# Optimization experiments

Hardware: AMD Instinct MI355X
Metric: run time of the kernel (lower is better)

Reference implementation:

```python
import jax, jax.numpy as jnp
import numpy as np

N_NODES = 50000
N_EDGES = 800000
IN_DIM = 768
HID = 32
HEADS = 4
OUT_DIM = 128


def setup_inputs() -> dict:
    key = jax.random.key(0)
    ks = jax.random.split(key, 7)
    h = jax.random.normal(ks[0], (N_NODES, IN_DIM), dtype=jnp.float32)
    W1 = jax.random.normal(ks[1], (HEADS, IN_DIM, HID), dtype=jnp.float32) * (1.0 / np.sqrt(IN_DIM))
    a1 = jax.random.normal(ks[2], (HEADS, 2 * HID), dtype=jnp.float32) * (1.0 / np.sqrt(2 * HID))
    W2 = jax.random.normal(ks[3], (1, HEADS * HID, OUT_DIM), dtype=jnp.float32) * (1.0 / np.sqrt(HEADS * HID))
    a2 = jax.random.normal(ks[4], (1, 2 * OUT_DIM), dtype=jnp.float32) * (1.0 / np.sqrt(2 * OUT_DIM))
    src = jax.random.randint(ks[5], (N_EDGES,), 0, N_NODES, dtype=jnp.int32)
    dst = jax.random.randint(ks[6], (N_EDGES,), 0, N_NODES, dtype=jnp.int32)
    return {"h": h, "W1": W1, "a1": a1, "W2": W2, "a2": a2, "src": src, "dst": dst}


def gat_layer(h, W, a, src, dst, n_nodes):
    # W: [H, Din, D], a: [H, 2D]; returns concat of heads: [N, H*D]
    z = jnp.einsum('ni,hio->nho', h, W)          # [N, H, D]
    D = z.shape[-1]
    a_src, a_dst = a[:, :D], a[:, D:]
    s_src = jnp.einsum('nhd,hd->nh', z, a_src)   # [N, H]
    s_dst = jnp.einsum('nhd,hd->nh', z, a_dst)
    e = jax.nn.leaky_relu(s_src[src] + s_dst[dst], 0.01)  # [E, H]
    # edge softmax over incoming edges of each dst node
    e_max = jax.ops.segment_max(e, dst, num_segments=n_nodes)
    e_max = jnp.where(jnp.isfinite(e_max), e_max, 0.0)     # empty segments -> -inf
    ex = jnp.exp(e - e_max[dst])
    denom = jax.ops.segment_sum(ex, dst, num_segments=n_nodes)
    alpha = ex / jnp.maximum(denom[dst], 1e-9)             # [E, H]
    msg = alpha[:, :, None] * z[src]                       # [E, H, D]
    out = jax.ops.segment_sum(msg, dst, num_segments=n_nodes)  # [N, H, D]
    return out.reshape(n_nodes, -1)


def reference(h, W1, a1, W2, a2, src, dst):
    n = h.shape[0]
    h1 = jax.nn.elu(gat_layer(h, W1, a1, src, dst, n))   # [N, HEADS*HID]
    h2 = gat_layer(h1, W2, a2, src, dst, n)              # [N, OUT_DIM]
    return h2
```

## Files before the change

### kernel.cpp

```cpp
#include <hip/hip_runtime.h>

#define NN 50000
#define NE 800000
#define IND 768
#define CH  128
#define NBLK 196
#define GBM 64
#define GBK 32
#define MBLKS 782

typedef __attribute__((ext_vector_type(8))) short bf16x8;
typedef __attribute__((ext_vector_type(4))) float f32x4;

__device__ __forceinline__ unsigned short bf16_rne(float f) {
    unsigned u = __float_as_uint(f);
    u += 0x7fffu + ((u >> 16) & 1u);
    return (unsigned short)(u >> 16);
}
__device__ __forceinline__ float bf16_to_f(unsigned short b) {
    return __uint_as_float(((unsigned)b) << 16);
}

__device__ __forceinline__ void cvt_split_pk(const float4& u0, const float4& u1,
                                             uint4& hi, uint4& lo)
{
    unsigned h0, h1, h2, h3;
    asm("v_cvt_pk_bf16_f32 %0, %1, %2" : "=v"(h0) : "v"(u0.x), "v"(u0.y));
    asm("v_cvt_pk_bf16_f32 %0, %1, %2" : "=v"(h1) : "v"(u0.z), "v"(u0.w));
    asm("v_cvt_pk_bf16_f32 %0, %1, %2" : "=v"(h2) : "v"(u1.x), "v"(u1.y));
    asm("v_cvt_pk_bf16_f32 %0, %1, %2" : "=v"(h3) : "v"(u1.z), "v"(u1.w));
    const float l0 = u0.x - __uint_as_float(h0 << 16);
    const float l1 = u0.y - __uint_as_float(h0 & 0xffff0000u);
    const float l2 = u0.z - __uint_as_float(h1 << 16);
    const float l3 = u0.w - __uint_as_float(h1 & 0xffff0000u);
    const float l4 = u1.x - __uint_as_float(h2 << 16);
    const float l5 = u1.y - __uint_as_float(h2 & 0xffff0000u);
    const float l6 = u1.z - __uint_as_float(h3 << 16);
    const float l7 = u1.w - __uint_as_float(h3 & 0xffff0000u);
    unsigned g0, g1, g2, g3;
    asm("v_cvt_pk_bf16_f32 %0, %1, %2" : "=v"(g0) : "v"(l0), "v"(l1));
    asm("v_cvt_pk_bf16_f32 %0, %1, %2" : "=v"(g1) : "v"(l2), "v"(l3));
    asm("v_cvt_pk_bf16_f32 %0, %1, %2" : "=v"(g2) : "v"(l4), "v"(l5));
    asm("v_cvt_pk_bf16_f32 %0, %1, %2" : "=v"(g3) : "v"(l6), "v"(l7));
    hi = make_uint4(h0, h1, h2, h3);
    lo = make_uint4(g0, g1, g2, g3);
}

__global__ void prep_b1(const float* __restrict__ W1,
                        unsigned short* __restrict__ Bhi, unsigned short* __restrict__ Blo)
{
    int idx = blockIdx.x * blockDim.x + threadIdx.x;
    if (idx >= CH * IND) return;
    int n = idx / IND, k = idx % IND;
    float v = W1[(size_t)(n >> 5) * IND * 32 + (size_t)k * 32 + (n & 31)];
    int kt = k >> 5, kk = k & 31, j = kk >> 3, e = kk & 7;
    int g = n * 4 + (j ^ ((n >> 1) & 3));
    int off = kt * 4096 + g * 8 + e;
    unsigned short hi = bf16_rne(v);
    float lo = v - bf16_to_f(hi);
    Bhi[off] = hi;
    Blo[off] = bf16_rne(lo);
}

__global__ void prep_b2(const float* __restrict__ W2,
                        unsigned short* __restrict__ Bhi, unsigned short* __restrict__ Blo)
{
    int idx = blockIdx.x * blockDim.x + threadIdx.x;
    if (idx >= CH * CH) return;
    int n = idx / CH, k = idx % CH;
    float v = W2[(size_t)k * CH + n];
    int kt = k >> 5, kk = k & 31, j = kk >> 3, e = kk & 7;
    int g = n * 4 + (j ^ ((n >> 1) & 3));
    int off = kt * 4096 + g * 8 + e;
    unsigned short hi = bf16_rne(v);
    float lo = v - bf16_to_f(hi);
    Bhi[off] = hi;
    Blo[off] = bf16_rne(lo);
}

template<int H>
__global__ __launch_bounds__(256) void gemm_fused(
    const float* __restrict__ A,
    const unsigned short* __restrict__ Bthi, const unsigned short* __restrict__ Btlo,
    const float* __restrict__ av,
    unsigned short* __restrict__ Z16,
    float* __restrict__ ss, float* __restrict__ sd, int K)
{
    __shared__ unsigned short Ahi[2048];
    __shared__ unsigned short Alo[2048];
    __shared__ unsigned short Bs[2][4096];
    __shared__ float sred[2][64][2];

    const int t = threadIdx.x;
    const int lane = t & 63;
    const int w = t >> 6;
    const int wr = w >> 1, wc = w & 1;
    const int lrow = lane & 15, kg = lane >> 4;
    const int m0 = blockIdx.x * GBM;
    const int nt = K >> 5;

    const int ar = t >> 2, aj = t & 3;
    const bool avalid = (m0 + ar) < NN;
    const float* aptr = A + (size_t)(avalid ? (m0 + ar) : 0) * K + aj * 8;
    const int ag8 = (ar * 4 + (aj ^ ((ar >> 1) & 3))) * 8;

    int aoff[2];
    #pragma unroll
    for (int mi = 0; mi < 2; ++mi) {
        const int r = wr * 32 + mi * 16 + lrow;
        aoff[mi] = (r * 4 + (kg ^ ((r >> 1) & 3))) * 8;
    }
    int boff[4];
    #pragma unroll
    for (int ni = 0; ni < 4; ++ni) {
        const int n = wc * 64 + ni * 16 + lrow;
        boff[ni] = (n * 4 + (kg ^ ((n >> 1) & 3))) * 8;
    }

    f32x4 acc[2][4];
    #pragma unroll
    for (int i = 0; i < 2; ++i)
        #pragma unroll
        for (int j = 0; j < 4; ++j) acc[i][j] = (f32x4)(0.f);

    for (int kt = 0; kt < nt; ++kt) {
        float4 v0 = make_float4(0.f, 0.f, 0.f, 0.f);
        float4 v1 = make_float4(0.f, 0.f, 0.f, 0.f);
        if (avalid) {
            const float* p = aptr + kt * GBK;
            v0 = *(const float4*)p;
            v1 = *(const float4*)(p + 4);
        }
        uint4 hi, lo;
        cvt_split_pk(v0, v1, hi, lo);
        __syncthreads();
        *(uint4*)&Ahi[ag8] = hi;
        *(uint4*)&Alo[ag8] = lo;
        #pragma unroll
        for (int i = 0; i < 4; ++i) {
            const int c = w * 4 + i;
            const int plane = c >> 3;
            const int co = (c & 7) * 512;
            const unsigned short* gs =
                (plane ? Btlo : Bthi) + (size_t)kt * 4096 + co + lane * 8;
            __builtin_amdgcn_global_load_lds(
                (const __attribute__((address_space(1))) unsigned int*)gs,
                (__attribute__((address_space(3))) unsigned int*)&Bs[plane][co],
                16, 0, 0);
        }
        __syncthreads();

        bf16x8 ahi[2], alo[2];
        #pragma unroll
        for (int mi = 0; mi < 2; ++mi) {
            ahi[mi] = *(const bf16x8*)&Ahi[aoff[mi]];
            alo[mi] = *(const bf16x8*)&Alo[aoff[mi]];
        }
        #pragma unroll
        for (int ni = 0; ni < 4; ++ni) {
            const bf16x8 bhi = *(const bf16x8*)&Bs[0][boff[ni]];
            const bf16x8 blo = *(const bf16x8*)&Bs[1][boff[ni]];
            #pragma unroll
            for (int mi = 0; mi < 2; ++mi) {
                acc[mi][ni] = __builtin_amdgcn_mfma_f32_16x16x32_bf16(ahi[mi], bhi, acc[mi][ni], 0, 0, 0);
                acc[mi][ni] = __builtin_amdgcn_mfma_f32_16x16x32_bf16(ahi[mi], blo, acc[mi][ni], 0, 0, 0);
                acc[mi][ni] = __builtin_amdgcn_mfma_f32_16x16x32_bf16(alo[mi], bhi, acc[mi][ni], 0, 0, 0);
            }
        }
    }

    const int NH = (H == 4) ? 2 : 1;
    float asc[4], adc[4];
    #pragma unroll
    for (int ni = 0; ni < 4; ++ni) {
        const int col = wc * 64 + ni * 16 + lrow;
        if (H == 4) {
            const int hh = col >> 5, d = col & 31;
            asc[ni] = av[hh * 64 + d];
            adc[ni] = av[hh * 64 + 32 + d];
        } else {
            asc[ni] = av[col];
            adc[ni] = av[128 + col];
        }
    }
    float es[2][4][2], ed[2][4][2];
    #pragma unroll
    for (int mi = 0; mi < 2; ++mi)
        #pragma unroll
        for (int j = 0; j < 4; ++j)
            #pragma unroll
            for (int q = 0; q < 2; ++q) { es[mi][j][q] = 0.f; ed[mi][j][q] = 0.f; }

    #pragma unroll
    for (int mi = 0; mi < 2; ++mi) {
        #pragma unroll
        for (int ni = 0; ni < 4; ++ni) {
            const int hh = (H == 4) ? (ni >> 1) : 0;
            const f32x4 a = acc[mi][ni];
            #pragma unroll
            for (int j = 0; j < 4; ++j) {
                es[mi][j][hh] = fmaf(a[j], asc[ni], es[mi][j][hh]);
                ed[mi][j][hh] = fmaf(a[j], adc[ni], ed[mi][j][hh]);
            }
        }
    }
    #pragma unroll
    for (int mi = 0; mi < 2; ++mi) {
        const int rbase = m0 + wr * 32 + mi * 16 + kg * 4;
        #pragma unroll
        for (int ni = 0; ni < 4; ++ni) {
            const int col = wc * 64 + ni * 16 + lrow;
            const f32x4 a = acc[mi][ni];
            #pragma unroll
            for (int j = 0; j < 4; ++j) {
                const int r = rbase + j;
                if (r < NN) Z16[(size_t)r * CH + col] = bf16_rne(a[j]);
            }
        }
    }
    #pragma unroll
    for (int off = 1; off < 16; off <<= 1) {
        #pragma unroll
        for (int mi = 0; mi < 2; ++mi)
            #pragma unroll
            for (int j = 0; j < 4; ++j)
                #pragma unroll
                for (int q = 0; q < NH; ++q) {
                    es[mi][j][q] += __shfl_xor(es[mi][j][q], off, 64);
                    ed[mi][j][q] += __shfl_xor(ed[mi][j][q], off, 64);
                }
    }
    if (H == 4) {
        if (lrow == 0) {
            #pragma unroll
            for (int mi = 0; mi < 2; ++mi)
                #pragma unroll
                for (int j = 0; j < 4; ++j) {
                    const int r = m0 + wr * 32 + mi * 16 + kg * 4 + j;
                    if (r < NN) {
                        #pragma unroll
                        for (int q = 0; q < 2; ++q) {
                            ss[r * 4 + wc * 2 + q] = es[mi][j][q];
                            sd[r * 4 + wc * 2 + q] = ed[mi][j][q];
                        }
                    }
                }
        }
    } else {
        if (lrow == 0) {
            #pragma unroll
            for (int mi = 0; mi < 2; ++mi)
                #pragma unroll
                for (int j = 0; j < 4; ++j) {
                    const int rl = wr * 32 + mi * 16 + kg * 4 + j;
                    sred[0][rl][wc] = es[mi][j][0];
                    sred[1][rl][wc] = ed[mi][j][0];
                }
        }
        __syncthreads();
        if (t < 64) {
            const int r = m0 + t;
            if (r < NN) {
                ss[r] = sred[0][t][0] + sred[0][t][1];
                sd[r] = sred[1][t][0] + sred[1][t][1];
            }
        }
    }
}

__global__ __launch_bounds__(256) void zero_cc(int* __restrict__ counts, int* __restrict__ cursor)
{
    int i = blockIdx.x * 256 + threadIdx.x;
    if (i < NN) { counts[i] = 0; cursor[i] = 0; }
}

__global__ void count_k(const int* __restrict__ dst, int* __restrict__ counts)
{
    int e = blockIdx.x * blockDim.x + threadIdx.x;
    if (e < NE) atomicAdd(&counts[dst[e]], 1);
}

__global__ __launch_bounds__(256) void scan1(const int* __restrict__ counts,
                                             int* __restrict__ exc, int* __restrict__ bsum)
{
    __shared__ int s[256];
    const int t = threadIdx.x;
    const int i = blockIdx.x * 256 + t;
    const int val = (i < NN) ? counts[i] : 0;
    s[t] = val;
    __syncthreads();
    #pragma unroll
    for (int off = 1; off < 256; off <<= 1) {
        int v = (t >= off) ? s[t - off] : 0;
        __syncthreads();
        s[t] += v;
        __syncthreads();
    }
    if (i < NN) exc[i] = s[t] - val;
    if (t == 255) bsum[blockIdx.x] = s[255];
}

__global__ __launch_bounds__(256) void scan2(const int* __restrict__ bsum,
                                             int* __restrict__ bexc)
{
    __shared__ int s[256];
    const int t = threadIdx.x;
    const int val = (t < NBLK) ? bsum[t] : 0;
    s[t] = val;
    __syncthreads();
    #pragma unroll
    for (int off = 1; off < 256; off <<= 1) {
        int v = (t >= off) ? s[t - off] : 0;
        __syncthreads();
        s[t] += v;
        __syncthreads();
    }
    bexc[t] = s[t] - val;
}

__global__ __launch_bounds__(256) void scan3(const int* __restrict__ exc,
                                             const int* __restrict__ bexc,
                                             int* __restrict__ offsets)
{
    const int i = blockIdx.x * 256 + threadIdx.x;
    if (i < NN) offsets[i] = exc[i] + bexc[i >> 8];
    if (i == 0) offsets[NN] = NE;
}

__global__ void scatter_es(const int* __restrict__ src, const int* __restrict__ dst,
                           const int* __restrict__ offsets, int* __restrict__ cursor,
                           int* __restrict__ es)
{
    int e = blockIdx.x * blockDim.x + threadIdx.x;
    if (e >= NE) return;
    int d = dst[e];
    int p = offsets[d] + atomicAdd(&cursor[d], 1);
    es[p] = src[e];
}

template<int H, bool ELU>
__global__ __launch_bounds__(256) void fused_agg(
    const int* __restrict__ offsets, const int* __restrict__ es,
    const float* __restrict__ s_src, const float* __restrict__ s_dst,
    const unsigned short* __restrict__ z16, float* __restrict__ out)
{
    const int wid = threadIdx.x >> 6;
    const int lane = threadIdx.x & 63;
    const int n = blockIdx.x * 4 + wid;
    const int beg = offsets[n], end = offsets[n + 1];
    const int deg = end - beg;

    __shared__ float alpha_sh[4][128][H];
    __shared__ int   es_sh[4][128];

    float sdv[H];
    #pragma unroll
    for (int h = 0; h < H; ++h) sdv[h] = s_dst[(size_t)n * H + h];

    const int myh = (H == 4) ? (lane >> 4) : 0;
    float m[H], ssum[H], inv[H];
    #pragma unroll
    for (int h = 0; h < H; ++h) { m[h] = -INFINITY; ssum[h] = 0.f; }
    float2 acc = make_float2(0.f, 0.f);

    if (deg <= 128) {
        for (int idx = lane; idx < deg; idx += 64) {
            const int s = es[beg + idx];
            es_sh[wid][idx] = s;
            if (H == 4) {
                const float4 sv = *(const float4*)&s_src[(size_t)s * 4];
                const float svv[4] = {sv.x, sv.y, sv.z, sv.w};
                float v4[4];
                #pragma unroll
                for (int h = 0; h < 4; ++h) {
                    float v = svv[h] + sdv[h];
                    v = v > 0.f ? v : 0.01f * v;
                    v4[h] = v;
                    const float mn = fmaxf(m[h], v);
                    ssum[h] = ssum[h] * __expf(m[h] - mn) + __expf(v - mn);
                    m[h] = mn;
                }
                *(float4*)&alpha_sh[wid][idx][0] = make_float4(v4[0], v4[1], v4[2], v4[3]);
            } else {
                float v = s_src[s] + sdv[0];
                v = v > 0.f ? v : 0.01f * v;
                alpha_sh[wid][idx][0] = v;
                const float mn = fmaxf(m[0], v);
                ssum[0] = ssum[0] * __expf(m[0] - mn) + __expf(v - mn);
                m[0] = mn;
            }
        }
        #pragma unroll
        for (int h = 0; h < H; ++h) {
            float mg = m[h];
            #pragma unroll
            for (int off = 1; off < 64; off <<= 1)
                mg = fmaxf(mg, __shfl_xor(mg, off, 64));
            float sg = ssum[h] * __expf(m[h] - mg);
            #pragma unroll
            for (int off = 1; off < 64; off <<= 1)
                sg += __shfl_xor(sg, off, 64);
            m[h] = mg;
            inv[h] = 1.0f / fmaxf(sg, 1e-9f);
        }
        for (int idx = lane; idx < deg; idx += 64) {
            #pragma unroll
            for (int h = 0; h < H; ++h)
                alpha_sh[wid][idx][h] = __expf(alpha_sh[wid][idx][h] - m[h]) * inv[h];
        }
        int j = 0;
        for (; j + 4 <= deg; j += 4) {
            const int s0 = es_sh[wid][j],     s1 = es_sh[wid][j + 1];
            const int s2 = es_sh[wid][j + 2], s3 = es_sh[wid][j + 3];
            const float a0 = alpha_sh[wid][j][myh],     a1 = alpha_sh[wid][j + 1][myh];
            const float a2 = alpha_sh[wid][j + 2][myh], a3 = alpha_sh[wid][j + 3][myh];
            const ushort2 u0 = *(const ushort2*)&z16[(size_t)s0 * CH + lane * 2];
            const ushort2 u1 = *(const ushort2*)&z16[(size_t)s1 * CH + lane * 2];
            const ushort2 u2 = *(const ushort2*)&z16[(size_t)s2 * CH + lane * 2];
            const ushort2 u3 = *(const ushort2*)&z16[(size_t)s3 * CH + lane * 2];
            acc.x = fmaf(a0, bf16_to_f(u0.x), acc.x); acc.y = fmaf(a0, bf16_to_f(u0.y), acc.y);
            acc.x = fmaf(a1, bf16_to_f(u1.x), acc.x); acc.y = fmaf(a1, bf16_to_f(u1.y), acc.y);
            acc.x = fmaf(a2, bf16_to_f(u2.x), acc.x); acc.y = fmaf(a2, bf16_to_f(u2.y), acc.y);
            acc.x = fmaf(a3, bf16_to_f(u3.x), acc.x); acc.y = fmaf(a3, bf16_to_f(u3.y), acc.y);
        }
        for (; j < deg; ++j) {
            const int s0 = es_sh[wid][j];
            const float a0 = alpha_sh[wid][j][myh];
            const ushort2 u0 = *(const ushort2*)&z16[(size_t)s0 * CH + lane * 2];
            acc.x = fmaf(a0, bf16_to_f(u0.x), acc.x); acc.y = fmaf(a0, bf16_to_f(u0.y), acc.y);
        }
    } else {
        for (int i = beg + lane; i < end; i += 64) {
            const int s = es[i];
            if (H == 4) {
                const float4 sv = *(const float4*)&s_src[(size_t)s * 4];
                const float svv[4] = {sv.x, sv.y, sv.z, sv.w};
                #pragma unroll
                for (int h = 0; h < 4; ++h) {
                    float v = svv[h] + sdv[h];
                    v = v > 0.f ? v : 0.01f * v;
                    const float mn = fmaxf(m[h], v);
                    ssum[h] = ssum[h] * __expf(m[h] - mn) + __expf(v - mn);
                    m[h] = mn;
                }
            } else {
                float v = s_src[s] + sdv[0];
                v = v > 0.f ? v : 0.01f * v;
                const float mn = fmaxf(m[0], v);
                ssum[0] = ssum[0] * __expf(m[0] - mn) + __expf(v - mn);
                m[0] = mn;
            }
        }
        #pragma unroll
        for (int h = 0; h < H; ++h) {
            float mg = m[h];
            #pragma unroll
            for (int off = 1; off < 64; off <<= 1)
                mg = fmaxf(mg, __shfl_xor(mg, off, 64));
            float sg = ssum[h] * __expf(m[h] - mg);
            #pragma unroll
            for (int off = 1; off < 64; off <<= 1)
                sg += __shfl_xor(sg, off, 64);
            m[h] = mg;
            inv[h] = 1.0f / fmaxf(sg, 1e-9f);
        }
        const int nch = (deg + 127) >> 7;
        for (int k = 0; k < nch; ++k) {
            const int base = beg + k * 128;
            int cnt = end - base;
            cnt = cnt < 0 ? 0 : (cnt > 128 ? 128 : cnt);
            for (int idx = lane; idx < cnt; idx += 64) {
                const int s = es[base + idx];
                es_sh[wid][idx] = s;
                if (H == 4) {
                    const float4 sv = *(const float4*)&s_src[(size_t)s * 4];
                    const float svv[4] = {sv.x, sv.y, sv.z, sv.w};
                    float a4[4];
                    #pragma unroll
                    for (int h = 0; h < 4; ++h) {
                        float v = svv[h] + sdv[h];
                        v = v > 0.f ? v : 0.01f * v;
                        a4[h] = __expf(v - m[h]) * inv[h];
                    }
                    *(float4*)&alpha_sh[wid][idx][0] = make_float4(a4[0], a4[1], a4[2], a4[3]);
                } else {
                    float v = s_src[s] + sdv[0];
                    v = v > 0.f ? v : 0.01f * v;
                    alpha_sh[wid][idx][0] = __expf(v - m[0]) * inv[0];
                }
            }
            for (int j = 0; j < cnt; ++j) {
                const int s0 = es_sh[wid][j];
                const float a0 = alpha_sh[wid][j][myh];
                const ushort2 u0 = *(const ushort2*)&z16[(size_t)s0 * CH + lane * 2];
                acc.x = fmaf(a0, bf16_to_f(u0.x), acc.x);
                acc.y = fmaf(a0, bf16_to_f(u0.y), acc.y);
            }
        }
    }

    if (ELU) {
        acc.x = acc.x > 0.f ? acc.x : expm1f(acc.x);
        acc.y = acc.y > 0.f ? acc.y : expm1f(acc.y);
    }
    *(float2*)&out[(size_t)n * CH + lane * 2] = acc;
}

extern "C" void kernel_launch(void* const* d_in, const int* in_sizes, int n_in,
                              void* d_out, int out_size, void* d_ws, size_t ws_size,
                              hipStream_t stream)
{
    const float* h   = (const float*)d_in[0];
    const float* W1  = (const float*)d_in[1];
    const float* a1  = (const float*)d_in[2];
    const float* W2  = (const float*)d_in[3];
    const float* a2  = (const float*)d_in[4];
    const int*   src = (const int*)d_in[5];
    const int*   dst = (const int*)d_in[6];
    float* out = (float*)d_out;

    char* ws = (char*)d_ws;
    unsigned short* Bthi1 = (unsigned short*)(ws + 0);
    unsigned short* Btlo1 = (unsigned short*)(ws + 196608);
    unsigned short* Bthi2 = (unsigned short*)(ws + 393216);
    unsigned short* Btlo2 = (unsigned short*)(ws + 425984);
    float* ss      = (float*)(ws + 458752);
    float* sd      = (float*)(ws + 1258752);
    int*   counts  = (int*)  (ws + 2058752);
    int*   exc     = (int*)  (ws + 2258752);
    int*   bsum    = (int*)  (ws + 2458752);
    int*   bexc    = (int*)  (ws + 2459776);
    int*   offsets = (int*)  (ws + 2460800);
    int*   cursor  = (int*)  (ws + 2661056);
    int*   es      = (int*)  (ws + 2861056);
    unsigned short* z16 = (unsigned short*)(ws + 6061056);
    float* h1      = (float*)(ws + 18861056);

    const int EB = 256;
    const int egrid = (NE + EB - 1) / EB;
    const int sgrid = NN / 4;

    zero_cc<<<NBLK, 256, 0, stream>>>(counts, cursor);
    count_k<<<egrid, EB, 0, stream>>>(dst, counts);
    scan1<<<NBLK, 256, 0, stream>>>(counts, exc, bsum);
    scan2<<<1, 256, 0, stream>>>(bsum, bexc);
    scan3<<<NBLK, 256, 0, stream>>>(exc, bexc, offsets);
    scatter_es<<<egrid, EB, 0, stream>>>(src, dst, offsets, cursor, es);

    prep_b1<<<(CH * IND + 255) / 256, 256, 0, stream>>>(W1, Bthi1, Btlo1);
    prep_b2<<<(CH * CH + 255) / 256, 256, 0, stream>>>(W2, Bthi2, Btlo2);

    gemm_fused<4><<<MBLKS, 256, 0, stream>>>(h, Bthi1, Btlo1, a1, z16, ss, sd, IND);
    fused_agg<4, true><<<sgrid, 256, 0, stream>>>(offsets, es, ss, sd, z16, h1);

    gemm_fused<1><<<MBLKS, 256, 0, stream>>>(h1, Bthi2, Btlo2, a2, z16, ss, sd, CH);
    fused_agg<1, false><<<sgrid, 256, 0, stream>>>(offsets, es, ss, sd, z16, out);
}
```

Measured before the change: 240.4 us.

## Process one destination node per half-wavefront with 4-channel vector gathers

The aggregation kernel now assigns each destination node to 32 lanes instead of a full 64-lane wavefront, so each block handles 8 nodes. Each lane gathers 4 bf16 channels (8 bytes) per source row instead of 2, and the softmax shuffle reductions shrink to 5 steps. The goal is to raise memory-level parallelism and cut the number of idle lanes on low-degree nodes (average degree is about 16). In exchange, shared memory per block doubles and per-lane loop work grows, and the two half-waves may diverge when node degrees differ.

```diff
diff --git a/kernel.cpp b/kernel.cpp
--- a/kernel.cpp
+++ b/kernel.cpp
@@ -344,29 +344,31 @@
     const float* __restrict__ s_src, const float* __restrict__ s_dst,
     const unsigned short* __restrict__ z16, float* __restrict__ out)
 {
-    const int wid = threadIdx.x >> 6;
     const int lane = threadIdx.x & 63;
-    const int n = blockIdx.x * 4 + wid;
+    const int hl = lane & 31;
+    const int slot = threadIdx.x >> 5;
+    const int n = blockIdx.x * 8 + slot;
     const int beg = offsets[n], end = offsets[n + 1];
     const int deg = end - beg;
 
-    __shared__ float alpha_sh[4][128][H];
-    __shared__ int   es_sh[4][128];
+    __shared__ float alpha_sh[8][128][H];
+    __shared__ int   es_sh[8][128];
 
     float sdv[H];
     #pragma unroll
     for (int h = 0; h < H; ++h) sdv[h] = s_dst[(size_t)n * H + h];
 
-    const int myh = (H == 4) ? (lane >> 4) : 0;
+    const int c0 = hl * 4;
+    const int myh = (H == 4) ? (c0 >> 5) : 0;
     float m[H], ssum[H], inv[H];
     #pragma unroll
     for (int h = 0; h < H; ++h) { m[h] = -INFINITY; ssum[h] = 0.f; }
-    float2 acc = make_float2(0.f, 0.f);
+    float4 acc = make_float4(0.f, 0.f, 0.f, 0.f);
 
     if (deg <= 128) {
-        for (int idx = lane; idx < deg; idx += 64) {
+        for (int idx = hl; idx < deg; idx += 32) {
             const int s = es[beg + idx];
-            es_sh[wid][idx] = s;
+            es_sh[slot][idx] = s;
             if (H == 4) {
                 const float4 sv = *(const float4*)&s_src[(size_t)s * 4];
                 const float svv[4] = {sv.x, sv.y, sv.z, sv.w};
@@ -380,11 +382,11 @@
                     ssum[h] = ssum[h] * __expf(m[h] - mn) + __expf(v - mn);
                     m[h] = mn;
                 }
-                *(float4*)&alpha_sh[wid][idx][0] = make_float4(v4[0], v4[1], v4[2], v4[3]);
+                *(float4*)&alpha_sh[slot][idx][0] = make_float4(v4[0], v4[1], v4[2], v4[3]);
             } else {
                 float v = s_src[s] + sdv[0];
                 v = v > 0.f ? v : 0.01f * v;
-                alpha_sh[wid][idx][0] = v;
+                alpha_sh[slot][idx][0] = v;
                 const float mn = fmaxf(m[0], v);
                 ssum[0] = ssum[0] * __expf(m[0] - mn) + __expf(v - mn);
                 m[0] = mn;
@@ -394,43 +396,48 @@
         for (int h = 0; h < H; ++h) {
             float mg = m[h];
             #pragma unroll
-            for (int off = 1; off < 64; off <<= 1)
+            for (int off = 1; off < 32; off <<= 1)
                 mg = fmaxf(mg, __shfl_xor(mg, off, 64));
             float sg = ssum[h] * __expf(m[h] - mg);
             #pragma unroll
-            for (int off = 1; off < 64; off <<= 1)
+            for (int off = 1; off < 32; off <<= 1)
                 sg += __shfl_xor(sg, off, 64);
             m[h] = mg;
             inv[h] = 1.0f / fmaxf(sg, 1e-9f);
         }
-        for (int idx = lane; idx < deg; idx += 64) {
+        for (int idx = hl; idx < deg; idx += 32) {
             #pragma unroll
             for (int h = 0; h < H; ++h)
-                alpha_sh[wid][idx][h] = __expf(alpha_sh[wid][idx][h] - m[h]) * inv[h];
+                alpha_sh[slot][idx][h] = __expf(alpha_sh[slot][idx][h] - m[h]) * inv[h];
         }
         int j = 0;
         for (; j + 4 <= deg; j += 4) {
-            const int s0 = es_sh[wid][j],     s1 = es_sh[wid][j + 1];
-            const int s2 = es_sh[wid][j + 2], s3 = es_sh[wid][j + 3];
-            const float a0 = alpha_sh[wid][j][myh],     a1 = alpha_sh[wid][j + 1][myh];
-            const float a2 = alpha_sh[wid][j + 2][myh], a3 = alpha_sh[wid][j + 3][myh];
-            const ushort2 u0 = *(const ushort2*)&z16[(size_t)s0 * CH + lane * 2];
-            const ushort2 u1 = *(const ushort2*)&z16[(size_t)s1 * CH + lane * 2];
-            const ushort2 u2 = *(const ushort2*)&z16[(size_t)s2 * CH + lane * 2];
-            const ushort2 u3 = *(const ushort2*)&z16[(size_t)s3 * CH + lane * 2];
+            const int s0 = es_sh[slot][j],     s1 = es_sh[slot][j + 1];
+            const int s2 = es_sh[slot][j + 2], s3 = es_sh[slot][j + 3];
+            const float a0 = alpha_sh[slot][j][myh],     a1 = alpha_sh[slot][j + 1][myh];
+            const float a2 = alpha_sh[slot][j + 2][myh], a3 = alpha_sh[slot][j + 3][myh];
+            const ushort4 u0 = *(const ushort4*)&z16[(size_t)s0 * CH + c0];
+            const ushort4 u1 = *(const ushort4*)&z16[(size_t)s1 * CH + c0];
+            const ushort4 u2 = *(const ushort4*)&z16[(size_t)s2 * CH + c0];
+            const ushort4 u3 = *(const ushort4*)&z16[(size_t)s3 * CH + c0];
             acc.x = fmaf(a0, bf16_to_f(u0.x), acc.x); acc.y = fmaf(a0, bf16_to_f(u0.y), acc.y);
+            acc.z = fmaf(a0, bf16_to_f(u0.z), acc.z); acc.w = fmaf(a0, bf16_to_f(u0.w), acc.w);
             acc.x = fmaf(a1, bf16_to_f(u1.x), acc.x); acc.y = fmaf(a1, bf16_to_f(u1.y), acc.y);
+            acc.z = fmaf(a1, bf16_to_f(u1.z), acc.z); acc.w = fmaf(a1, bf16_to_f(u1.w), acc.w);
             acc.x = fmaf(a2, bf16_to_f(u2.x), acc.x); acc.y = fmaf(a2, bf16_to_f(u2.y), acc.y);
+            acc.z = fmaf(a2, bf16_to_f(u2.z), acc.z); acc.w = fmaf(a2, bf16_to_f(u2.w), acc.w);
             acc.x = fmaf(a3, bf16_to_f(u3.x), acc.x); acc.y = fmaf(a3, bf16_to_f(u3.y), acc.y);
+            acc.z = fmaf(a3, bf16_to_f(u3.z), acc.z); acc.w = fmaf(a3, bf16_to_f(u3.w), acc.w);
         }
         for (; j < deg; ++j) {
-            const int s0 = es_sh[wid][j];
-            const float a0 = alpha_sh[wid][j][myh];
-            const ushort2 u0 = *(const ushort2*)&z16[(size_t)s0 * CH + lane * 2];
+            const int s0 = es_sh[slot][j];
+            const float a0 = alpha_sh[slot][j][myh];
+            const ushort4 u0 = *(const ushort4*)&z16[(size_t)s0 * CH + c0];
             acc.x = fmaf(a0, bf16_to_f(u0.x), acc.x); acc.y = fmaf(a0, bf16_to_f(u0.y), acc.y);
+            acc.z = fmaf(a0, bf16_to_f(u0.z), acc.z); acc.w = fmaf(a0, bf16_to_f(u0.w), acc.w);
         }
     } else {
-        for (int i = beg + lane; i < end; i += 64) {
+        for (int i = beg + hl; i < end; i += 32) {
             const int s = es[i];
             if (H == 4) {
                 const float4 sv = *(const float4*)&s_src[(size_t)s * 4];
@@ -455,11 +462,11 @@
         for (int h = 0; h < H; ++h) {
             float mg = m[h];
             #pragma unroll
-            for (int off = 1; off < 64; off <<= 1)
+            for (int off = 1; off < 32; off <<= 1)
                 mg = fmaxf(mg, __shfl_xor(mg, off, 64));
             float sg = ssum[h] * __expf(m[h] - mg);
             #pragma unroll
-            for (int off = 1; off < 64; off <<= 1)
+            for (int off = 1; off < 32; off <<= 1)
                 sg += __shfl_xor(sg, off, 64);
             m[h] = mg;
             inv[h] = 1.0f / fmaxf(sg, 1e-9f);
@@ -469,9 +476,9 @@
             const int base = beg + k * 128;
             int cnt = end - base;
             cnt = cnt < 0 ? 0 : (cnt > 128 ? 128 : cnt);
-            for (int idx = lane; idx < cnt; idx += 64) {
+            for (int idx = hl; idx < cnt; idx += 32) {
                 const int s = es[base + idx];
-                es_sh[wid][idx] = s;
+                es_sh[slot][idx] = s;
                 if (H == 4) {
                     const float4 sv = *(const float4*)&s_src[(size_t)s * 4];
                     const float svv[4] = {sv.x, sv.y, sv.z, sv.w};
@@ -482,19 +489,19 @@
                         v = v > 0.f ? v : 0.01f * v;
                         a4[h] = __expf(v - m[h]) * inv[h];
                     }
-                    *(float4*)&alpha_sh[wid][idx][0] = make_float4(a4[0], a4[1], a4[2], a4[3]);
+                    *(float4*)&alpha_sh[slot][idx][0] = make_float4(a4[0], a4[1], a4[2], a4[3]);
                 } else {
                     float v = s_src[s] + sdv[0];
                     v = v > 0.f ? v : 0.01f * v;
-                    alpha_sh[wid][idx][0] = __expf(v - m[0]) * inv[0];
+                    alpha_sh[slot][idx][0] = __expf(v - m[0]) * inv[0];
                 }
             }
             for (int j = 0; j < cnt; ++j) {
-                const int s0 = es_sh[wid][j];
-                const float a0 = alpha_sh[wid][j][myh];
-                const ushort2 u0 = *(const ushort2*)&z16[(size_t)s0 * CH + lane * 2];
-                acc.x = fmaf(a0, bf16_to_f(u0.x), acc.x);
-                acc.y = fmaf(a0, bf16_to_f(u0.y), acc.y);
+                const int s0 = es_sh[slot][j];
+                const float a0 = alpha_sh[slot][j][myh];
+                const ushort4 u0 = *(const ushort4*)&z16[(size_t)s0 * CH + c0];
+                acc.x = fmaf(a0, bf16_to_f(u0.x), acc.x); acc.y = fmaf(a0, bf16_to_f(u0.y), acc.y);
+                acc.z = fmaf(a0, bf16_to_f(u0.z), acc.z); acc.w = fmaf(a0, bf16_to_f(u0.w), acc.w);
             }
         }
     }
@@ -502,8 +509,10 @@
     if (ELU) {
         acc.x = acc.x > 0.f ? acc.x : expm1f(acc.x);
         acc.y = acc.y > 0.f ? acc.y : expm1f(acc.y);
-    }
-    *(float2*)&out[(size_t)n * CH + lane * 2] = acc;
+        acc.z = acc.z > 0.f ? acc.z : expm1f(acc.z);
+        acc.w = acc.w > 0.f ? acc.w : expm1f(acc.w);
+    }
+    *(float4*)&out[(size_t)n * CH + c0] = acc;
 }
 
 extern "C" void kernel_launch(void* const* d_in, const int* in_sizes, int n_in,
@@ -538,7 +547,7 @@
 
     const int EB = 256;
     const int egrid = (NE + EB - 1) / EB;
-    const int sgrid = NN / 4;
+    const int agrid = NN / 8;
 
     zero_cc<<<NBLK, 256, 0, stream>>>(counts, cursor);
     count_k<<<egrid, EB, 0, stream>>>(dst, counts);
@@ -551,8 +560,8 @@
     prep_b2<<<(CH * CH + 255) / 256, 256, 0, stream>>>(W2, Bthi2, Btlo2);
 
     gemm_fused<4><<<MBLKS, 256, 0, stream>>>(h, Bthi1, Btlo1, a1, z16, ss, sd, IND);
-    fused_agg<4, true><<<sgrid, 256, 0, stream>>>(offsets, es, ss, sd, z16, h1);
+    fused_agg<4, true><<<agrid, 256, 0, stream>>>(offsets, es, ss, sd, z16, h1);
 
     gemm_fused<1><<<MBLKS, 256, 0, stream>>>(h1, Bthi2, Btlo2, a2, z16, ss, sd, CH);
-    fused_agg<1, false><<<sgrid, 256, 0, stream>>>(offsets, es, ss, sd, z16, out);
-}
+    fused_agg<1, false><<<agrid, 256, 0, stream>>>(offsets, es, ss, sd, z16, out);
+}
```

Measured after the change: 235.1 us. 1.02x faster.
